# Kernel tuning notes

Measured on AMD Instinct MI355X. Metric: run time of the kernel, lower is better.

Reference implementation:

```python
import jax, jax.numpy as jnp
import numpy as np

FORGET_BIAS = 1.0

def _lstm_step(c, h, x, W, b):
    # TF BasicLSTMCell: concat([x, h]) @ W + b -> split into i, j, f, o
    gates = jnp.concatenate([x, h], axis=-1) @ W + b
    i, j, f, o = jnp.split(gates, 4, axis=-1)
    new_c = c * jax.nn.sigmoid(f + FORGET_BIAS) + jax.nn.sigmoid(i) * jnp.tanh(j)
    new_h = jnp.tanh(new_c) * jax.nn.sigmoid(o)
    return new_c, new_h

def setup_inputs() -> dict:
    key = jax.random.key(0)
    ks = jax.random.split(key, 8)
    B, T, D, H, C = 64, 128, 2048, 512, 101
    s1 = 1.0 / np.sqrt(D + H)
    s2 = 1.0 / np.sqrt(2 * H)
    so = 1.0 / np.sqrt(H)
    return {
        "inputs": jax.random.normal(ks[0], (B, T, D), dtype=jnp.float32),
        "labels": jax.random.randint(ks[1], (B, T), 0, C, dtype=jnp.int64),
        "W1": jax.random.normal(ks[2], (D + H, 4 * H), dtype=jnp.float32) * s1,
        "b1": jnp.zeros((4 * H,), dtype=jnp.float32),
        "W2": jax.random.normal(ks[3], (2 * H, 4 * H), dtype=jnp.float32) * s2,
        "b2": jnp.zeros((4 * H,), dtype=jnp.float32),
        "Wout": jax.random.normal(ks[4], (H, C), dtype=jnp.float32) * so,
        "bout": jnp.zeros((C,), dtype=jnp.float32),
    }

def reference(inputs, labels, W1, b1, W2, b2, Wout, bout):
    B, T, D = inputs.shape
    H = Wout.shape[0]

    def step(carry, x_t):
        (c1, h1), (c2, h2) = carry
        c1, h1 = _lstm_step(c1, h1, x_t, W1, b1)
        c2, h2 = _lstm_step(c2, h2, h1, W2, b2)
        return ((c1, h1), (c2, h2)), h2

    zeros = jnp.zeros((B, H), dtype=inputs.dtype)
    init = ((zeros, zeros), (zeros, zeros))
    xs = jnp.swapaxes(inputs, 0, 1)  # [T, B, D]
    _, hs = jax.lax.scan(step, init, xs)  # hs: [T, B, H]
    outputs = jnp.swapaxes(hs, 0, 1)  # [B, T, H]

    logits = outputs @ Wout + bout  # [B, T, C]
    preds = jax.nn.softmax(logits, axis=-1)
    log_probs = jax.nn.log_softmax(logits, axis=-1)
    ce = -jnp.take_along_axis(log_probs, labels[..., None], axis=-1)[..., 0]  # [B, T]
    cost = jnp.mean(jnp.sum(ce, axis=1))
    return preds, cost
```

## Files before the change

### kernel.cpp

```cpp
#include <hip/hip_runtime.h>
#include <cmath>

#define Bb   64
#define Tt   128
#define Dd   2048
#define Hh   512
#define Gg   2048
#define Cc   101
#define ROWS 8192

typedef unsigned short u16;
typedef __attribute__((ext_vector_type(8))) short bf16x8;
typedef __attribute__((ext_vector_type(4))) float f32x4;

__device__ __forceinline__ u16 bf16rne(float x) {
  unsigned u = __float_as_uint(x);
  unsigned r = (u + 0x7fffu + ((u >> 16) & 1u)) >> 16;
  return (u16)r;
}
__device__ __forceinline__ void split_bf16(float x, u16& h, u16& l) {
  h = bf16rne(x);
  l = bf16rne(x - __uint_as_float(((unsigned)h) << 16));
}
__device__ __forceinline__ float sigm(float x) { return 1.f / (1.f + expf(-x)); }

__global__ __launch_bounds__(256)
void convert_hilo(const float* __restrict__ src, u16* __restrict__ hi,
                  u16* __restrict__ lo, int n4) {
  for (int i = blockIdx.x * 256 + threadIdx.x; i < n4; i += gridDim.x * 256) {
    const float4 v = ((const float4*)src)[i];
    ushort4 h, l;
    split_bf16(v.x, h.x, l.x);
    split_bf16(v.y, h.y, l.y);
    split_bf16(v.z, h.z, l.z);
    split_bf16(v.w, h.w, l.w);
    ((ushort4*)hi)[i] = h;
    ((ushort4*)lo)[i] = l;
  }
}

__global__ __launch_bounds__(256)
void convertT_w1(const float* __restrict__ W1, u16* __restrict__ Th,
                 u16* __restrict__ Tl) {
  __shared__ float tl[32][33];
  const int tx = threadIdx.x, ty = threadIdx.y;
  const int k0 = blockIdx.x * 32, c0 = blockIdx.y * 32;
#pragma unroll
  for (int j = 0; j < 4; ++j)
    tl[ty + j * 8][tx] = W1[(size_t)(k0 + ty + j * 8) * Gg + (c0 + tx)];
  __syncthreads();
#pragma unroll
  for (int j = 0; j < 4; ++j) {
    const float v = tl[tx][ty + j * 8];
    u16 h, l;
    split_bf16(v, h, l);
    const size_t o = (size_t)(c0 + ty + j * 8) * Dd + (k0 + tx);
    Th[o] = h;
    Tl[o] = l;
  }
}

__global__ __launch_bounds__(256)
void permuteW(const float* __restrict__ src, u16* __restrict__ dh,
              u16* __restrict__ dl, int K) {
  __shared__ float tl[32][33];
  const int tx = threadIdx.x, ty = threadIdx.y;
  const int k0 = blockIdx.x * 32, c0 = blockIdx.y * 32;
#pragma unroll
  for (int j = 0; j < 4; ++j)
    tl[ty + j * 8][tx] = src[(size_t)(k0 + ty + j * 8) * Gg + (c0 + tx)];
  __syncthreads();
#pragma unroll
  for (int j = 0; j < 4; ++j) {
    const int col = c0 + ty + j * 8;
    const int g = col >> 9, mg = col & 511;
    const int cg = mg >> 2, m = mg & 3;
    const float v = tl[tx][ty + j * 8];
    u16 h, l;
    split_bf16(v, h, l);
    const size_t o = (size_t)(cg * 16 + g * 4 + m) * K + k0 + tx;
    dh[o] = h;
    dl[o] = l;
  }
}

__global__ __launch_bounds__(256)
void gemm1_mfma(const u16* __restrict__ Ah, const u16* __restrict__ Al,
                const u16* __restrict__ Bh, const u16* __restrict__ Bl,
                const float* __restrict__ bias, float* __restrict__ C) {
  __shared__ u16 Ash[128][40];
  __shared__ u16 Asl[128][40];
  __shared__ u16 Bsh[128][40];
  __shared__ u16 Bsl[128][40];
  const int tid  = threadIdx.x;
  const int lane = tid & 63, wave = tid >> 6;
  const int wm = wave >> 1, wn = wave & 1;
  const int l15 = lane & 15, k8 = (lane >> 4) * 8, r4 = (lane >> 4) * 4;
  const int row0 = blockIdx.y * 128, col0 = blockIdx.x * 128;
  const int srow = tid >> 1, sk = (tid & 1) * 16;

  const u16* pAh = Ah + (size_t)(row0 + srow) * Dd + sk;
  const u16* pAl = Al + (size_t)(row0 + srow) * Dd + sk;
  const u16* pBh = Bh + (size_t)(col0 + srow) * Dd + sk;
  const u16* pBl = Bl + (size_t)(col0 + srow) * Dd + sk;

  f32x4 acc[4][4];
#pragma unroll
  for (int i = 0; i < 4; ++i)
#pragma unroll
    for (int j = 0; j < 4; ++j) acc[i][j] = (f32x4){0.f, 0.f, 0.f, 0.f};

  for (int k0 = 0; k0 < Dd; k0 += 32) {
    *(bf16x8*)(&Ash[srow][sk])     = *(const bf16x8*)(pAh + k0);
    *(bf16x8*)(&Ash[srow][sk + 8]) = *(const bf16x8*)(pAh + k0 + 8);
    *(bf16x8*)(&Asl[srow][sk])     = *(const bf16x8*)(pAl + k0);
    *(bf16x8*)(&Asl[srow][sk + 8]) = *(const bf16x8*)(pAl + k0 + 8);
    *(bf16x8*)(&Bsh[srow][sk])     = *(const bf16x8*)(pBh + k0);
    *(bf16x8*)(&Bsh[srow][sk + 8]) = *(const bf16x8*)(pBh + k0 + 8);
    *(bf16x8*)(&Bsl[srow][sk])     = *(const bf16x8*)(pBl + k0);
    *(bf16x8*)(&Bsl[srow][sk + 8]) = *(const bf16x8*)(pBl + k0 + 8);
    __syncthreads();

    bf16x8 afh[4], afl[4], bfh[4], bfl[4];
#pragma unroll
    for (int mt = 0; mt < 4; ++mt) {
      afh[mt] = *(const bf16x8*)(&Ash[wm * 64 + mt * 16 + l15][k8]);
      afl[mt] = *(const bf16x8*)(&Asl[wm * 64 + mt * 16 + l15][k8]);
    }
#pragma unroll
    for (int nt = 0; nt < 4; ++nt) {
      bfh[nt] = *(const bf16x8*)(&Bsh[wn * 64 + nt * 16 + l15][k8]);
      bfl[nt] = *(const bf16x8*)(&Bsl[wn * 64 + nt * 16 + l15][k8]);
    }
#pragma unroll
    for (int mt = 0; mt < 4; ++mt)
#pragma unroll
      for (int nt = 0; nt < 4; ++nt) {
        acc[mt][nt] = __builtin_amdgcn_mfma_f32_16x16x32_bf16(
            afh[mt], bfh[nt], acc[mt][nt], 0, 0, 0);
        acc[mt][nt] = __builtin_amdgcn_mfma_f32_16x16x32_bf16(
            afh[mt], bfl[nt], acc[mt][nt], 0, 0, 0);
        acc[mt][nt] = __builtin_amdgcn_mfma_f32_16x16x32_bf16(
            afl[mt], bfh[nt], acc[mt][nt], 0, 0, 0);
      }
    __syncthreads();
  }

#pragma unroll
  for (int nt = 0; nt < 4; ++nt) {
    const int col = col0 + wn * 64 + nt * 16 + l15;
    const float bj = bias[col];
#pragma unroll
    for (int mt = 0; mt < 4; ++mt) {
      float* Cp = C + (size_t)(row0 + wm * 64 + mt * 16 + r4) * Gg + col;
#pragma unroll
      for (int r = 0; r < 4; ++r)
        Cp[(size_t)r * Gg] = acc[mt][nt][r] + bj;
    }
  }
}

#define BM 128
#define BN 128
#define BK 16

__global__ __launch_bounds__(256)
void sgemm_bias(const float* __restrict__ A, const float* __restrict__ B,
                const float* __restrict__ bias, float* __restrict__ C,
                int M, int N, int K) {
  __shared__ float As[BK][BM];
  __shared__ float Bs[BK][BN];
  const int tid  = threadIdx.x;
  const int row0 = blockIdx.y * BM, col0 = blockIdx.x * BN;
  const int tr = (tid >> 4) << 3;
  const int tc = (tid & 15) << 3;

  float acc[8][8];
#pragma unroll
  for (int i = 0; i < 8; ++i)
#pragma unroll
    for (int j = 0; j < 8; ++j) acc[i][j] = 0.f;

  const int arow = tid >> 1;
  const int acol = (tid & 1) << 3;
  const int brow = tid >> 4;
  const int bcol = (tid & 15) << 3;
  const float* Ap = A + (size_t)(row0 + arow) * K + acol;
  const float* Bp = B + (size_t)brow * N + (col0 + bcol);

  for (int k0 = 0; k0 < K; k0 += BK) {
    const float4 a0 = *(const float4*)(Ap + k0);
    const float4 a1 = *(const float4*)(Ap + k0 + 4);
    const float4 bv0 = *(const float4*)(Bp + (size_t)k0 * N);
    const float4 bv1 = *(const float4*)(Bp + (size_t)k0 * N + 4);
    As[acol + 0][arow] = a0.x;
    As[acol + 1][arow] = a0.y;
    As[acol + 2][arow] = a0.z;
    As[acol + 3][arow] = a0.w;
    As[acol + 4][arow] = a1.x;
    As[acol + 5][arow] = a1.y;
    As[acol + 6][arow] = a1.z;
    As[acol + 7][arow] = a1.w;
    *(float4*)(&Bs[brow][bcol])     = bv0;
    *(float4*)(&Bs[brow][bcol + 4]) = bv1;
    __syncthreads();
#pragma unroll
    for (int k = 0; k < BK; ++k) {
      float a[8], b[8];
      *(float4*)(a)     = *(const float4*)(&As[k][tr]);
      *(float4*)(a + 4) = *(const float4*)(&As[k][tr + 4]);
      *(float4*)(b)     = *(const float4*)(&Bs[k][tc]);
      *(float4*)(b + 4) = *(const float4*)(&Bs[k][tc + 4]);
#pragma unroll
      for (int i = 0; i < 8; ++i)
#pragma unroll
        for (int j = 0; j < 8; ++j)
          acc[i][j] = fmaf(a[i], b[j], acc[i][j]);
    }
    __syncthreads();
  }

  float bj[8];
#pragma unroll
  for (int j = 0; j < 8; ++j) bj[j] = bias[col0 + tc + j];
#pragma unroll
  for (int i = 0; i < 8; ++i) {
    float* Cp = C + (size_t)(row0 + tr + i) * N + (col0 + tc);
    float4 o0, o1;
    o0.x = acc[i][0] + bj[0]; o0.y = acc[i][1] + bj[1];
    o0.z = acc[i][2] + bj[2]; o0.w = acc[i][3] + bj[3];
    o1.x = acc[i][4] + bj[4]; o1.y = acc[i][5] + bj[5];
    o1.z = acc[i][6] + bj[6]; o1.w = acc[i][7] + bj[7];
    *(float4*)(Cp)     = o0;
    *(float4*)(Cp + 4) = o1;
  }
}

__device__ __forceinline__ void mm_half(
    const u16* __restrict__ hh_src, const u16* __restrict__ hl_src,
    const u16* __restrict__ wph, const u16* __restrict__ wpl, int Kw,
    f32x4& acc, u16 (*Ah)[64][136], u16 (*Al)[64][136],
    u16 (*Bh)[16][136], u16 (*Bl)[16][136], int tid, int lane, int w) {
  const int hr = tid >> 2, hk = (tid & 3) * 32;
  const int wv = tid >> 4, wk = (tid & 15) * 8;
  const int fr = lane & 15, f8 = (lane >> 4) * 8;

  bf16x8 rh[4], rl[4], rwh, rwl;
#pragma unroll
  for (int j = 0; j < 4; ++j) {
    rh[j] = *(const bf16x8*)(hh_src + hr * 512 + hk + j * 8);
    rl[j] = *(const bf16x8*)(hl_src + hr * 512 + hk + j * 8);
  }
  rwh = *(const bf16x8*)(wph + (size_t)wv * Kw + wk);
  rwl = *(const bf16x8*)(wpl + (size_t)wv * Kw + wk);
#pragma unroll
  for (int j = 0; j < 4; ++j) {
    *(bf16x8*)&Ah[0][hr][hk + j * 8] = rh[j];
    *(bf16x8*)&Al[0][hr][hk + j * 8] = rl[j];
  }
  *(bf16x8*)&Bh[0][wv][wk] = rwh;
  *(bf16x8*)&Bl[0][wv][wk] = rwl;
  __syncthreads();

  for (int kc = 0; kc < 4; ++kc) {
    const int cur = kc & 1;
    if (kc < 3) {
      const int ko = (kc + 1) * 128;
#pragma unroll
      for (int j = 0; j < 4; ++j) {
        rh[j] = *(const bf16x8*)(hh_src + hr * 512 + ko + hk + j * 8);
        rl[j] = *(const bf16x8*)(hl_src + hr * 512 + ko + hk + j * 8);
      }
      rwh = *(const bf16x8*)(wph + (size_t)wv * Kw + ko + wk);
      rwl = *(const bf16x8*)(wpl + (size_t)wv * Kw + ko + wk);
    }
#pragma unroll
    for (int s = 0; s < 4; ++s) {
      const bf16x8 afh = *(const bf16x8*)&Ah[cur][w * 16 + fr][s * 32 + f8];
      const bf16x8 afl = *(const bf16x8*)&Al[cur][w * 16 + fr][s * 32 + f8];
      const bf16x8 bfh = *(const bf16x8*)&Bh[cur][fr][s * 32 + f8];
      const bf16x8 bfl = *(const bf16x8*)&Bl[cur][fr][s * 32 + f8];
      acc = __builtin_amdgcn_mfma_f32_16x16x32_bf16(afh, bfh, acc, 0, 0, 0);
      acc = __builtin_amdgcn_mfma_f32_16x16x32_bf16(afh, bfl, acc, 0, 0, 0);
      acc = __builtin_amdgcn_mfma_f32_16x16x32_bf16(afl, bfh, acc, 0, 0, 0);
    }
    if (kc < 3) {
      const int nb = cur ^ 1;
#pragma unroll
      for (int j = 0; j < 4; ++j) {
        *(bf16x8*)&Ah[nb][hr][hk + j * 8] = rh[j];
        *(bf16x8*)&Al[nb][hr][hk + j * 8] = rl[j];
      }
      *(bf16x8*)&Bh[nb][wv][wk] = rwh;
      *(bf16x8*)&Bl[nb][wv][wk] = rwl;
    }
    __syncthreads();
  }
}

__global__ __launch_bounds__(256, 1)
void fused_step2(const float* __restrict__ pre,
                 const u16* __restrict__ WP1h, const u16* __restrict__ WP1l,
                 const u16* __restrict__ WP2h, const u16* __restrict__ WP2l,
                 const float* __restrict__ b2,
                 u16* __restrict__ h1hi, u16* __restrict__ h1lo,
                 u16* __restrict__ h2hi, u16* __restrict__ h2lo,
                 float* __restrict__ h2all,
                 float* __restrict__ c1, float* __restrict__ c2, int t) {
  __shared__ u16 Ah[2][64][136], Al[2][64][136];
  __shared__ u16 Bh[2][16][136], Bl[2][16][136];
  __shared__ float ex[4][16][17];
  const int tid = threadIdx.x;
  const int lane = tid & 63, w = tid >> 6;
  const int fr = lane & 15;
  const bool isL2 = blockIdx.x >= 128;
  const int cg = blockIdx.x & 127;

  f32x4 acc = {0.f, 0.f, 0.f, 0.f};
  bool have = false;

  if (!isL2) {
    if (t >= Tt) return;
    if (t > 0) {
      const int sl = (t - 1) & 1;
      mm_half(h1hi + (sl << 15), h1lo + (sl << 15),
              WP1h + (size_t)cg * 16 * 512, WP1l + (size_t)cg * 16 * 512, 512,
              acc, Ah, Al, Bh, Bl, tid, lane, w);
      have = true;
    }
  } else {
    if (t < 1) return;
    const u16* ph = WP2h + (size_t)cg * 16 * 1024;
    const u16* pl = WP2l + (size_t)cg * 16 * 1024;
    {
      const int sl = (t - 1) & 1;
      mm_half(h1hi + (sl << 15), h1lo + (sl << 15), ph, pl, 1024,
              acc, Ah, Al, Bh, Bl, tid, lane, w);
    }
    if (t >= 2) {
      const int sl = (t - 2) & 1;
      mm_half(h2hi + (sl << 15), h2lo + (sl << 15), ph + 512, pl + 512, 1024,
              acc, Ah, Al, Bh, Bl, tid, lane, w);
    }
    have = true;
  }

  if (have) {
#pragma unroll
    for (int r = 0; r < 4; ++r)
      ex[w][(lane >> 4) * 4 + r][fr] = acc[r];
  }
  __syncthreads();

  const int b = tid >> 2, m = tid & 3;
  float s0 = 0.f, s1 = 0.f, s2 = 0.f, s3 = 0.f;
  if (have) {
    s0 = ex[b >> 4][b & 15][0 + m];
    s1 = ex[b >> 4][b & 15][4 + m];
    s2 = ex[b >> 4][b & 15][8 + m];
    s3 = ex[b >> 4][b & 15][12 + m];
  }
  const int col = cg * 4 + m;
  const int ci = b * Hh + col;
  if (!isL2) {
    const float* pp = pre + ((size_t)b * Tt + t) * Gg + col;
    const float gi = pp[0] + s0, gj = pp[512] + s1;
    const float gf = pp[1024] + s2, go = pp[1536] + s3;
    const float cp = (t > 0) ? c1[ci] : 0.f;
    const float nc = fmaf(cp, sigm(gf + 1.f), sigm(gi) * tanhf(gj));
    c1[ci] = nc;
    const float nh = tanhf(nc) * sigm(go);
    u16 hh, hl;
    split_bf16(nh, hh, hl);
    const int hidx = ((t & 1) << 15) + ci;
    h1hi[hidx] = hh;
    h1lo[hidx] = hl;
  } else {
    const float gi = b2[col] + s0, gj = b2[512 + col] + s1;
    const float gf = b2[1024 + col] + s2, go = b2[1536 + col] + s3;
    const float cp = (t >= 2) ? c2[ci] : 0.f;
    const float nc = fmaf(cp, sigm(gf + 1.f), sigm(gi) * tanhf(gj));
    c2[ci] = nc;
    const float nh = tanhf(nc) * sigm(go);
    h2all[((size_t)b * Tt + (t - 1)) * Hh + col] = nh;
    u16 hh, hl;
    split_bf16(nh, hh, hl);
    const int hidx = (((t - 1) & 1) << 15) + ci;
    h2hi[hidx] = hh;
    h2lo[hidx] = hl;
  }
}

__global__ __launch_bounds__(128)
void proj_softmax(const float* __restrict__ h2, const float* __restrict__ Wout,
                  const float* __restrict__ bout, const int* __restrict__ labels,
                  float* __restrict__ preds, float* __restrict__ ce) {
  __shared__ float hs[8][Hh];
  __shared__ float wred[2][2];
  const int tid = threadIdx.x;
  const int wid = tid >> 6;
  const int r0  = blockIdx.x * 8;

  for (int i = tid; i < 8 * (Hh / 4); i += 128) {
    const int row = i >> 7;
    const int c4  = i & 127;
    ((float4*)hs[row])[c4] =
        ((const float4*)(h2 + ((size_t)(r0 + row) * Hh)))[c4];
  }
  __syncthreads();

  const bool act = (tid < Cc);
  float acc[8];
  {
    const float bj = act ? bout[tid] : 0.f;
#pragma unroll
    for (int i = 0; i < 8; ++i) acc[i] = bj;
  }
  if (act) {
#pragma unroll 4
    for (int k = 0; k < Hh; ++k) {
      const float w = Wout[k * Cc + tid];
#pragma unroll
      for (int i = 0; i < 8; ++i) acc[i] = fmaf(hs[i][k], w, acc[i]);
    }
  }

  for (int row = 0; row < 8; ++row) {
    const float v = act ? acc[row] : -INFINITY;
    float mw = v;
#pragma unroll
    for (int off = 32; off > 0; off >>= 1) mw = fmaxf(mw, __shfl_xor(mw, off));
    if ((tid & 63) == 0) wred[0][wid] = mw;
    __syncthreads();
    const float mx = fmaxf(wred[0][0], wred[0][1]);
    const float e = act ? expf(v - mx) : 0.f;
    float sw = e;
#pragma unroll
    for (int off = 32; off > 0; off >>= 1) sw += __shfl_xor(sw, off);
    if ((tid & 63) == 0) wred[1][wid] = sw;
    __syncthreads();
    const float sum = wred[1][0] + wred[1][1];
    if (act) preds[(size_t)(r0 + row) * Cc + tid] = e / sum;
    const int lab = labels[r0 + row];
    if (tid == lab) ce[r0 + row] = logf(sum) + mx - v;
    __syncthreads();
  }
}

__global__ __launch_bounds__(256)
void reduce_cost(const float* __restrict__ ce, float* __restrict__ out) {
  __shared__ float red[256];
  const int tid = threadIdx.x;
  float s = 0.f;
  for (int i = tid; i < ROWS; i += 256) s += ce[i];
  red[tid] = s;
  __syncthreads();
  for (int st = 128; st > 0; st >>= 1) {
    if (tid < st) red[tid] += red[tid + st];
    __syncthreads();
  }
  if (tid == 0) out[0] = red[0] / (float)Bb;
}

extern "C" void kernel_launch(void* const* d_in, const int* in_sizes, int n_in,
                              void* d_out, int out_size, void* d_ws, size_t ws_size,
                              hipStream_t stream) {
  const float* inputs = (const float*)d_in[0];
  const int*   labels = (const int*)d_in[1];
  const float* W1     = (const float*)d_in[2];
  const float* b1     = (const float*)d_in[3];
  const float* W2     = (const float*)d_in[4];
  const float* b2     = (const float*)d_in[5];
  const float* Wout   = (const float*)d_in[6];
  const float* bout   = (const float*)d_in[7];
  float* out = (float*)d_out;

  float* ws    = (float*)d_ws;
  float* pre   = ws;
  float* h2all = pre   + (size_t)ROWS * Gg;
  float* c1    = h2all + (size_t)ROWS * Hh;
  float* c2    = c1    + (size_t)Bb * Hh;
  float* ceb   = c2    + (size_t)Bb * Hh;
  u16* h1hi = (u16*)(ceb + ROWS);
  u16* h1lo = h1hi + 2 * 64 * 512;
  u16* h2hi = h1lo + 2 * 64 * 512;
  u16* h2lo = h2hi + 2 * 64 * 512;
  u16* WP1h = h2lo + 2 * 64 * 512;
  u16* WP1l = WP1h + 128 * 16 * 512;
  u16* WP2h = WP1l + 128 * 16 * 512;
  u16* WP2l = WP2h + 128 * 16 * 1024;
  u16* Xhi  = WP2l + 128 * 16 * 1024;
  u16* Xlo  = Xhi  + (size_t)ROWS * Dd;
  u16* W1Th = Xlo  + (size_t)ROWS * Dd;
  u16* W1Tl = W1Th + (size_t)Gg * Dd;
  const size_t need = (size_t)((char*)(W1Tl + (size_t)Gg * Dd) - (char*)d_ws);
  const bool use_mfma = ws_size >= need;

  permuteW<<<dim3(16, 64), dim3(32, 8), 0, stream>>>(
      W1 + (size_t)Dd * Gg, WP1h, WP1l, 512);
  permuteW<<<dim3(32, 64), dim3(32, 8), 0, stream>>>(W2, WP2h, WP2l, 1024);

  if (use_mfma) {
    convert_hilo<<<2048, 256, 0, stream>>>(inputs, Xhi, Xlo, ROWS * Dd / 4);
    convertT_w1<<<dim3(64, 64), dim3(32, 8), 0, stream>>>(W1, W1Th, W1Tl);
    gemm1_mfma<<<dim3(Gg / 128, ROWS / 128), 256, 0, stream>>>(
        Xhi, Xlo, W1Th, W1Tl, b1, pre);
  } else {
    sgemm_bias<<<dim3(Gg / BN, ROWS / BM), dim3(256), 0, stream>>>(
        inputs, W1, b1, pre, ROWS, Gg, Dd);
  }

  for (int t = 0; t <= Tt; ++t)
    fused_step2<<<256, 256, 0, stream>>>(pre, WP1h, WP1l, WP2h, WP2l, b2,
                                         h1hi, h1lo, h2hi, h2lo,
                                         h2all, c1, c2, t);

  proj_softmax<<<ROWS / 8, 128, 0, stream>>>(h2all, Wout, bout, labels, out, ceb);
  reduce_cost<<<1, 256, 0, stream>>>(ceb, out + (size_t)ROWS * Cc);
}
```

Baseline: 1.822 ms.

## Move output projection to split-bf16 MFMA GEMM and pipeline layer-2 recurrent matmul

The output projection now runs as a split-bf16 MFMA GEMM over hi/lo bf16 copies of h2 and a transposed, padded Wout, instead of a scalar FMA loop. Softmax and cross-entropy move to a separate one-wave-per-row kernel. The layer-2 recurrent step replaces two sequential mm_half calls with one fused, register-prefetched, double-buffered loop over both h1 and h2 K-chunks. This adds a logits buffer, extra launches and more workspace, and the bf16 split may change accuracy slightly.

```diff
diff --git a/kernel.cpp b/kernel.cpp
--- a/kernel.cpp
+++ b/kernel.cpp
@@ -7,6 +7,7 @@
 #define Hh   512
 #define Gg   2048
 #define Cc   101
+#define PC   112
 #define ROWS 8192
 
 typedef unsigned short u16;
@@ -57,6 +58,19 @@
     const size_t o = (size_t)(c0 + ty + j * 8) * Dd + (k0 + tx);
     Th[o] = h;
     Tl[o] = l;
+  }
+}
+
+__global__ __launch_bounds__(256)
+void convert_woutT(const float* __restrict__ Wout, u16* __restrict__ Th,
+                   u16* __restrict__ Tl) {
+  const int c = blockIdx.x;
+  for (int k = threadIdx.x; k < Hh; k += 256) {
+    const float v = (c < Cc) ? Wout[k * Cc + c] : 0.f;
+    u16 h, l;
+    split_bf16(v, h, l);
+    Th[c * Hh + k] = h;
+    Tl[c * Hh + k] = l;
   }
 }
 
@@ -158,6 +172,107 @@
         Cp[(size_t)r * Gg] = acc[mt][nt][r] + bj;
     }
   }
+}
+
+__global__ __launch_bounds__(256)
+void gemm_proj(const u16* __restrict__ Ah, const u16* __restrict__ Al,
+               const u16* __restrict__ Bh, const u16* __restrict__ Bl,
+               const float* __restrict__ bout, float* __restrict__ logits) {
+  __shared__ u16 Ash[128][40];
+  __shared__ u16 Asl[128][40];
+  __shared__ u16 Bsh[PC][40];
+  __shared__ u16 Bsl[PC][40];
+  const int tid  = threadIdx.x;
+  const int lane = tid & 63, wave = tid >> 6;
+  const int l15 = lane & 15, k8 = (lane >> 4) * 8, r4 = (lane >> 4) * 4;
+  const int row0 = blockIdx.x * 128;
+  const int srow = tid >> 1, sk = (tid & 1) * 16;
+
+  const u16* pAh = Ah + (size_t)(row0 + srow) * Hh + sk;
+  const u16* pAl = Al + (size_t)(row0 + srow) * Hh + sk;
+  const u16* pBh = Bh + (size_t)srow * Hh + sk;
+  const u16* pBl = Bl + (size_t)srow * Hh + sk;
+
+  f32x4 acc[2][7];
+#pragma unroll
+  for (int i = 0; i < 2; ++i)
+#pragma unroll
+    for (int j = 0; j < 7; ++j) acc[i][j] = (f32x4){0.f, 0.f, 0.f, 0.f};
+
+  for (int k0 = 0; k0 < Hh; k0 += 32) {
+    *(bf16x8*)(&Ash[srow][sk])     = *(const bf16x8*)(pAh + k0);
+    *(bf16x8*)(&Ash[srow][sk + 8]) = *(const bf16x8*)(pAh + k0 + 8);
+    *(bf16x8*)(&Asl[srow][sk])     = *(const bf16x8*)(pAl + k0);
+    *(bf16x8*)(&Asl[srow][sk + 8]) = *(const bf16x8*)(pAl + k0 + 8);
+    if (srow < PC) {
+      *(bf16x8*)(&Bsh[srow][sk])     = *(const bf16x8*)(pBh + k0);
+      *(bf16x8*)(&Bsh[srow][sk + 8]) = *(const bf16x8*)(pBh + k0 + 8);
+      *(bf16x8*)(&Bsl[srow][sk])     = *(const bf16x8*)(pBl + k0);
+      *(bf16x8*)(&Bsl[srow][sk + 8]) = *(const bf16x8*)(pBl + k0 + 8);
+    }
+    __syncthreads();
+
+    bf16x8 afh[2], afl[2], bfh[7], bfl[7];
+#pragma unroll
+    for (int mt = 0; mt < 2; ++mt) {
+      afh[mt] = *(const bf16x8*)(&Ash[wave * 32 + mt * 16 + l15][k8]);
+      afl[mt] = *(const bf16x8*)(&Asl[wave * 32 + mt * 16 + l15][k8]);
+    }
+#pragma unroll
+    for (int nt = 0; nt < 7; ++nt) {
+      bfh[nt] = *(const bf16x8*)(&Bsh[nt * 16 + l15][k8]);
+      bfl[nt] = *(const bf16x8*)(&Bsl[nt * 16 + l15][k8]);
+    }
+#pragma unroll
+    for (int mt = 0; mt < 2; ++mt)
+#pragma unroll
+      for (int nt = 0; nt < 7; ++nt) {
+        acc[mt][nt] = __builtin_amdgcn_mfma_f32_16x16x32_bf16(
+            afh[mt], bfh[nt], acc[mt][nt], 0, 0, 0);
+        acc[mt][nt] = __builtin_amdgcn_mfma_f32_16x16x32_bf16(
+            afh[mt], bfl[nt], acc[mt][nt], 0, 0, 0);
+        acc[mt][nt] = __builtin_amdgcn_mfma_f32_16x16x32_bf16(
+            afl[mt], bfh[nt], acc[mt][nt], 0, 0, 0);
+      }
+    __syncthreads();
+  }
+
+#pragma unroll
+  for (int nt = 0; nt < 7; ++nt) {
+    const int col = nt * 16 + l15;
+    const float bj = (col < Cc) ? bout[col] : 0.f;
+#pragma unroll
+    for (int mt = 0; mt < 2; ++mt) {
+      float* Lp = logits + (size_t)(row0 + wave * 32 + mt * 16 + r4) * PC + col;
+#pragma unroll
+      for (int r = 0; r < 4; ++r)
+        Lp[(size_t)r * PC] = acc[mt][nt][r] + bj;
+    }
+  }
+}
+
+__global__ __launch_bounds__(256)
+void softmax_ce(const float* __restrict__ logits, const int* __restrict__ labels,
+                float* __restrict__ preds, float* __restrict__ ce) {
+  const int lane = threadIdx.x & 63, wv = threadIdx.x >> 6;
+  const int row = blockIdx.x * 4 + wv;
+  const float* lg = logits + (size_t)row * PC;
+  const bool a0 = (lane < Cc), a1 = (lane + 64 < Cc);
+  const float v0 = a0 ? lg[lane] : -INFINITY;
+  const float v1 = a1 ? lg[lane + 64] : -INFINITY;
+  float m = fmaxf(v0, v1);
+#pragma unroll
+  for (int off = 32; off > 0; off >>= 1) m = fmaxf(m, __shfl_xor(m, off));
+  const float e0 = a0 ? expf(v0 - m) : 0.f;
+  const float e1 = a1 ? expf(v1 - m) : 0.f;
+  float s = e0 + e1;
+#pragma unroll
+  for (int off = 32; off > 0; off >>= 1) s += __shfl_xor(s, off);
+  if (a0) preds[(size_t)row * Cc + lane] = e0 / s;
+  if (a1) preds[(size_t)row * Cc + lane + 64] = e1 / s;
+  const int lab = labels[row];
+  if (lab == lane)           ce[row] = logf(s) + m - v0;
+  else if (lab == lane + 64) ce[row] = logf(s) + m - v1;
 }
 
 #define BM 128
@@ -305,7 +420,7 @@
                  const float* __restrict__ b2,
                  u16* __restrict__ h1hi, u16* __restrict__ h1lo,
                  u16* __restrict__ h2hi, u16* __restrict__ h2lo,
-                 float* __restrict__ h2all,
+                 u16* __restrict__ h2fh, u16* __restrict__ h2fl,
                  float* __restrict__ c1, float* __restrict__ c2, int t) {
   __shared__ u16 Ah[2][64][136], Al[2][64][136];
   __shared__ u16 Bh[2][16][136], Bl[2][16][136];
@@ -330,17 +445,73 @@
     }
   } else {
     if (t < 1) return;
+    const u16* A1h = h1hi + (((t - 1) & 1) << 15);
+    const u16* A1l = h1lo + (((t - 1) & 1) << 15);
+    const u16* A2h = h2hi + (((t - 2) & 1) << 15);
+    const u16* A2l = h2lo + (((t - 2) & 1) << 15);
     const u16* ph = WP2h + (size_t)cg * 16 * 1024;
     const u16* pl = WP2l + (size_t)cg * 16 * 1024;
-    {
-      const int sl = (t - 1) & 1;
-      mm_half(h1hi + (sl << 15), h1lo + (sl << 15), ph, pl, 1024,
-              acc, Ah, Al, Bh, Bl, tid, lane, w);
-    }
-    if (t >= 2) {
-      const int sl = (t - 2) & 1;
-      mm_half(h2hi + (sl << 15), h2lo + (sl << 15), ph + 512, pl + 512, 1024,
-              acc, Ah, Al, Bh, Bl, tid, lane, w);
+    const bool h2ok = (t >= 2);
+
+    const int hr = tid >> 2, hk = (tid & 3) * 32;
+    const int wv = tid >> 4, wk = (tid & 15) * 8;
+    const int f8 = (lane >> 4) * 8;
+
+    bf16x8 rh[4], rl[4], rwh, rwl;
+#pragma unroll
+    for (int j = 0; j < 4; ++j) {
+      rh[j] = *(const bf16x8*)(A1h + hr * 512 + hk + j * 8);
+      rl[j] = *(const bf16x8*)(A1l + hr * 512 + hk + j * 8);
+    }
+    rwh = *(const bf16x8*)(ph + (size_t)wv * 1024 + wk);
+    rwl = *(const bf16x8*)(pl + (size_t)wv * 1024 + wk);
+#pragma unroll
+    for (int j = 0; j < 4; ++j) {
+      *(bf16x8*)&Ah[0][hr][hk + j * 8] = rh[j];
+      *(bf16x8*)&Al[0][hr][hk + j * 8] = rl[j];
+    }
+    *(bf16x8*)&Bh[0][wv][wk] = rwh;
+    *(bf16x8*)&Bl[0][wv][wk] = rwl;
+    __syncthreads();
+
+    for (int kc = 0; kc < 8; ++kc) {
+      const int cur = kc & 1;
+      if (kc < 7) {
+        const int nk = kc + 1;
+        const u16* sh = (nk < 4) ? A1h : A2h;
+        const u16* sl2 = (nk < 4) ? A1l : A2l;
+        const int ko = (nk & 3) * 128;
+#pragma unroll
+        for (int j = 0; j < 4; ++j) {
+          rh[j] = *(const bf16x8*)(sh + hr * 512 + ko + hk + j * 8);
+          rl[j] = *(const bf16x8*)(sl2 + hr * 512 + ko + hk + j * 8);
+        }
+        rwh = *(const bf16x8*)(ph + (size_t)wv * 1024 + nk * 128 + wk);
+        rwl = *(const bf16x8*)(pl + (size_t)wv * 1024 + nk * 128 + wk);
+      }
+      if (kc < 4 || h2ok) {
+#pragma unroll
+        for (int s = 0; s < 4; ++s) {
+          const bf16x8 afh = *(const bf16x8*)&Ah[cur][w * 16 + fr][s * 32 + f8];
+          const bf16x8 afl = *(const bf16x8*)&Al[cur][w * 16 + fr][s * 32 + f8];
+          const bf16x8 bfh = *(const bf16x8*)&Bh[cur][fr][s * 32 + f8];
+          const bf16x8 bfl = *(const bf16x8*)&Bl[cur][fr][s * 32 + f8];
+          acc = __builtin_amdgcn_mfma_f32_16x16x32_bf16(afh, bfh, acc, 0, 0, 0);
+          acc = __builtin_amdgcn_mfma_f32_16x16x32_bf16(afh, bfl, acc, 0, 0, 0);
+          acc = __builtin_amdgcn_mfma_f32_16x16x32_bf16(afl, bfh, acc, 0, 0, 0);
+        }
+      }
+      if (kc < 7) {
+        const int nb = cur ^ 1;
+#pragma unroll
+        for (int j = 0; j < 4; ++j) {
+          *(bf16x8*)&Ah[nb][hr][hk + j * 8] = rh[j];
+          *(bf16x8*)&Al[nb][hr][hk + j * 8] = rl[j];
+        }
+        *(bf16x8*)&Bh[nb][wv][wk] = rwh;
+        *(bf16x8*)&Bl[nb][wv][wk] = rwl;
+      }
+      __syncthreads();
     }
     have = true;
   }
@@ -382,68 +553,14 @@
     const float nc = fmaf(cp, sigm(gf + 1.f), sigm(gi) * tanhf(gj));
     c2[ci] = nc;
     const float nh = tanhf(nc) * sigm(go);
-    h2all[((size_t)b * Tt + (t - 1)) * Hh + col] = nh;
     u16 hh, hl;
     split_bf16(nh, hh, hl);
     const int hidx = (((t - 1) & 1) << 15) + ci;
     h2hi[hidx] = hh;
     h2lo[hidx] = hl;
-  }
-}
-
-__global__ __launch_bounds__(128)
-void proj_softmax(const float* __restrict__ h2, const float* __restrict__ Wout,
-                  const float* __restrict__ bout, const int* __restrict__ labels,
-                  float* __restrict__ preds, float* __restrict__ ce) {
-  __shared__ float hs[8][Hh];
-  __shared__ float wred[2][2];
-  const int tid = threadIdx.x;
-  const int wid = tid >> 6;
-  const int r0  = blockIdx.x * 8;
-
-  for (int i = tid; i < 8 * (Hh / 4); i += 128) {
-    const int row = i >> 7;
-    const int c4  = i & 127;
-    ((float4*)hs[row])[c4] =
-        ((const float4*)(h2 + ((size_t)(r0 + row) * Hh)))[c4];
-  }
-  __syncthreads();
-
-  const bool act = (tid < Cc);
-  float acc[8];
-  {
-    const float bj = act ? bout[tid] : 0.f;
-#pragma unroll
-    for (int i = 0; i < 8; ++i) acc[i] = bj;
-  }
-  if (act) {
-#pragma unroll 4
-    for (int k = 0; k < Hh; ++k) {
-      const float w = Wout[k * Cc + tid];
-#pragma unroll
-      for (int i = 0; i < 8; ++i) acc[i] = fmaf(hs[i][k], w, acc[i]);
-    }
-  }
-
-  for (int row = 0; row < 8; ++row) {
-    const float v = act ? acc[row] : -INFINITY;
-    float mw = v;
-#pragma unroll
-    for (int off = 32; off > 0; off >>= 1) mw = fmaxf(mw, __shfl_xor(mw, off));
-    if ((tid & 63) == 0) wred[0][wid] = mw;
-    __syncthreads();
-    const float mx = fmaxf(wred[0][0], wred[0][1]);
-    const float e = act ? expf(v - mx) : 0.f;
-    float sw = e;
-#pragma unroll
-    for (int off = 32; off > 0; off >>= 1) sw += __shfl_xor(sw, off);
-    if ((tid & 63) == 0) wred[1][wid] = sw;
-    __syncthreads();
-    const float sum = wred[1][0] + wred[1][1];
-    if (act) preds[(size_t)(r0 + row) * Cc + tid] = e / sum;
-    const int lab = labels[r0 + row];
-    if (tid == lab) ce[r0 + row] = logf(sum) + mx - v;
-    __syncthreads();
+    const size_t fo = ((size_t)b * Tt + (t - 1)) * Hh + col;
+    h2fh[fo] = hh;
+    h2fl[fo] = hl;
   }
 }
 
@@ -475,21 +592,25 @@
   const float* bout   = (const float*)d_in[7];
   float* out = (float*)d_out;
 
-  float* ws    = (float*)d_ws;
-  float* pre   = ws;
-  float* h2all = pre   + (size_t)ROWS * Gg;
-  float* c1    = h2all + (size_t)ROWS * Hh;
-  float* c2    = c1    + (size_t)Bb * Hh;
-  float* ceb   = c2    + (size_t)Bb * Hh;
-  u16* h1hi = (u16*)(ceb + ROWS);
+  float* ws     = (float*)d_ws;
+  float* pre    = ws;
+  float* c1     = pre    + (size_t)ROWS * Gg;
+  float* c2     = c1     + (size_t)Bb * Hh;
+  float* ceb    = c2     + (size_t)Bb * Hh;
+  float* logits = ceb    + ROWS;
+  u16* h1hi = (u16*)(logits + (size_t)ROWS * PC);
   u16* h1lo = h1hi + 2 * 64 * 512;
   u16* h2hi = h1lo + 2 * 64 * 512;
   u16* h2lo = h2hi + 2 * 64 * 512;
-  u16* WP1h = h2lo + 2 * 64 * 512;
+  u16* h2fh = h2lo + 2 * 64 * 512;
+  u16* h2fl = h2fh + (size_t)ROWS * Hh;
+  u16* WP1h = h2fl + (size_t)ROWS * Hh;
   u16* WP1l = WP1h + 128 * 16 * 512;
   u16* WP2h = WP1l + 128 * 16 * 512;
   u16* WP2l = WP2h + 128 * 16 * 1024;
-  u16* Xhi  = WP2l + 128 * 16 * 1024;
+  u16* WoTh = WP2l + 128 * 16 * 1024;
+  u16* WoTl = WoTh + PC * Hh;
+  u16* Xhi  = WoTl + PC * Hh;
   u16* Xlo  = Xhi  + (size_t)ROWS * Dd;
   u16* W1Th = Xlo  + (size_t)ROWS * Dd;
   u16* W1Tl = W1Th + (size_t)Gg * Dd;
@@ -499,6 +620,7 @@
   permuteW<<<dim3(16, 64), dim3(32, 8), 0, stream>>>(
       W1 + (size_t)Dd * Gg, WP1h, WP1l, 512);
   permuteW<<<dim3(32, 64), dim3(32, 8), 0, stream>>>(W2, WP2h, WP2l, 1024);
+  convert_woutT<<<PC, 256, 0, stream>>>(Wout, WoTh, WoTl);
 
   if (use_mfma) {
     convert_hilo<<<2048, 256, 0, stream>>>(inputs, Xhi, Xlo, ROWS * Dd / 4);
@@ -513,8 +635,9 @@
   for (int t = 0; t <= Tt; ++t)
     fused_step2<<<256, 256, 0, stream>>>(pre, WP1h, WP1l, WP2h, WP2l, b2,
                                          h1hi, h1lo, h2hi, h2lo,
-                                         h2all, c1, c2, t);
-
-  proj_softmax<<<ROWS / 8, 128, 0, stream>>>(h2all, Wout, bout, labels, out, ceb);
+                                         h2fh, h2fl, c1, c2, t);
+
+  gemm_proj<<<ROWS / 128, 256, 0, stream>>>(h2fh, h2fl, WoTh, WoTl, bout, logits);
+  softmax_ce<<<ROWS / 4, 256, 0, stream>>>(logits, labels, out, ceb);
   reduce_cost<<<1, 256, 0, stream>>>(ceb, out + (size_t)ROWS * Cc);
 }
```

New measurement: 1.783 ms. 1.02x faster.
